# Optimization experiments

Hardware: AMD Instinct MI355X
Metric: run time of the kernel (lower is better)

## Reference

```python
import jax, jax.numpy as jnp
import numpy as np

B, T, F, H = 32768, 64, 8, 16
NUM_LABELS, OUT_WIN = 4, 8
FC1_OUT = F * T          # 512
FC2_OUT = NUM_LABELS * OUT_WIN  # 32


def _lstm_relu(x_tbf, W, U, b):
    """Keras LSTM with activation='relu', recurrent_activation='sigmoid'.
    x_tbf: [T, B, F_in]. Returns all hidden states [T, B, H].
    Gate order in Keras kernel: i, f, c, o."""
    Bv = x_tbf.shape[1]
    h0 = jnp.zeros((Bv, H), x_tbf.dtype)
    c0 = jnp.zeros((Bv, H), x_tbf.dtype)

    def step(carry, xt):
        h, c = carry
        z = xt @ W + h @ U + b  # [B, 4H]
        i, f, g, o = jnp.split(z, 4, axis=-1)
        i = jax.nn.sigmoid(i)
        f = jax.nn.sigmoid(f)
        o = jax.nn.sigmoid(o)
        c = f * c + i * jax.nn.relu(g)
        h = o * jax.nn.relu(c)
        return (h, c), h

    _, hs = jax.lax.scan(step, (h0, c0), x_tbf)
    return hs  # [T, B, H]


def setup_inputs() -> dict:
    key = jax.random.key(0)
    ks = jax.random.split(key, 12)
    s = lambda fan_in: 1.0 / np.sqrt(fan_in)
    x = jax.random.normal(ks[0], (B, T, F), dtype=jnp.float32)
    W1 = jax.random.normal(ks[1], (F, 4 * H), dtype=jnp.float32) * s(F)
    U1 = jax.random.normal(ks[2], (H, 4 * H), dtype=jnp.float32) * s(H)
    b1 = jnp.zeros((4 * H,), jnp.float32)
    W2 = jax.random.normal(ks[3], (H, 4 * H), dtype=jnp.float32) * s(H)
    U2 = jax.random.normal(ks[4], (H, 4 * H), dtype=jnp.float32) * s(H)
    b2 = jnp.zeros((4 * H,), jnp.float32)
    Wfc1 = jax.random.normal(ks[5], (H, FC1_OUT), dtype=jnp.float32) * s(H)
    bfc1 = jnp.zeros((FC1_OUT,), jnp.float32)
    Wfc2 = jax.random.normal(ks[6], (FC1_OUT, FC2_OUT), dtype=jnp.float32) * s(FC1_OUT)
    bfc2 = jnp.zeros((FC2_OUT,), jnp.float32)
    return {"x": x, "W1": W1, "U1": U1, "b1": b1, "W2": W2, "U2": U2,
            "b2": b2, "Wfc1": Wfc1, "bfc1": bfc1, "Wfc2": Wfc2, "bfc2": bfc2}


def reference(x, W1, U1, b1, W2, U2, b2, Wfc1, bfc1, Wfc2, bfc2):
    x_tbf = jnp.transpose(x, (1, 0, 2))        # [T, B, F]
    h1 = _lstm_relu(x_tbf, W1, U1, b1)         # [T, B, H] (return_sequences=True)
    h2 = _lstm_relu(h1, W2, U2, b2)[-1]        # [B, H] (return_sequences=False)
    # Dropout is identity at inference (training=False).
    y = jax.nn.relu(h2 @ Wfc1 + bfc1)          # [B, 512]
    y = y @ Wfc2 + bfc2                        # [B, 32]
    return y
```

## Files before the change

### kernel.cpp

```cpp
#include <hip/hip_runtime.h>
#include <stdint.h>


#define NT 64
#define NF 8

typedef __attribute__((ext_vector_type(8))) short bf16x8;
typedef __attribute__((ext_vector_type(4))) float f32x4;

#define MFMA16 __builtin_amdgcn_mfma_f32_16x16x32_bf16

static __device__ __forceinline__ short f2bf(float f) {
  uint32_t u = __float_as_uint(f);
  u += 0x7FFFu + ((u >> 16) & 1u);
  return (short)(u >> 16);
}
static __device__ __forceinline__ float bf2f(short s) {
  return __uint_as_float(((uint32_t)(uint16_t)s) << 16);
}
static __device__ __forceinline__ void split_hl(float f, short& hi, short& lo) {
  short h = f2bf(f);
  hi = h;
  lo = f2bf(f - bf2f(h));
}
static __device__ __forceinline__ float sigmoidf_(float v) {
  return __builtin_amdgcn_rcpf(1.0f + __expf(-v));
}
static __device__ __forceinline__ void lds_fence() {
  asm volatile("s_waitcnt lgkmcnt(0)" ::: "memory");
  __builtin_amdgcn_sched_barrier(0);
}

__global__ __launch_bounds__(256, 2) void lstm_fused(
    const float* __restrict__ x,
    const float* __restrict__ W1, const float* __restrict__ U1, const float* __restrict__ b1,
    const float* __restrict__ W2, const float* __restrict__ U2, const float* __restrict__ b2,
    const float* __restrict__ Wfc1, const float* __restrict__ bfc1,
    const float* __restrict__ Wfc2, const float* __restrict__ bfc2,
    float* __restrict__ out)
{
  const int tid  = threadIdx.x;
  const int lane = tid & 63;
  const int wv   = tid >> 6;
  const int col  = lane & 15;
  const int g    = lane >> 4;
  const int ho   = (g & 1) * 8;
  const int base = (blockIdx.x * 4 + wv) * 16;

  __shared__ __align__(16) short lds_all[4][1536 + 1280];
  short* const s1_hi = &lds_all[wv][0];
  short* const s1_lo = s1_hi + 384;
  short* const s2_hi = s1_hi + 768;
  short* const s2_lo = s1_hi + 1152;
  short* const c_hi  = s1_hi + 1536;
  short* const c_lo  = s1_hi + 1536 + 640;

  for (int i = lane; i < 1536; i += 64) s1_hi[i] = 0;
  lds_fence();

  bf16x8 B1a[4], B2a[4], B1b[4], B2b[4];
#pragma unroll
  for (int n = 0; n < 4; ++n) {
    const int c = 16 * n + col;
#pragma unroll
    for (int j = 0; j < 8; ++j) {
      const int k = 8 * g + j;
      short h, l;
      if (k < 8)       { split_hl(W1[k * 64 + c], h, l);        B1a[n][j] = h; B2a[n][j] = l; }
      else if (k < 16) { split_hl(W1[(k - 8) * 64 + c], h, l);  B1a[n][j] = h; B2a[n][j] = 0; }
      else             { split_hl(U1[(k - 16) * 64 + c], h, l); B1a[n][j] = h; B2a[n][j] = l; }
      short h2, l2;
      if (k < 16) split_hl(W2[k * 64 + c], h2, l2);
      else        split_hl(U2[(k - 16) * 64 + c], h2, l2);
      B1b[n][j] = h2; B2b[n][j] = l2;
    }
  }

  float bias1[4], bias2[4];
#pragma unroll
  for (int n = 0; n < 4; ++n) { bias1[n] = b1[16 * n + col]; bias2[n] = b2[16 * n + col]; }

  f32x4 c1 = {0.f, 0.f, 0.f, 0.f};
  f32x4 c2 = {0.f, 0.f, 0.f, 0.f};

  const float* xrow = x + (size_t)(base + col) * (NT * NF);
  const short* const l2ph = (g < 2) ? s1_hi : s2_hi;
  const short* const l2pl = (g < 2) ? s1_lo : s2_lo;

  for (int t = 0; t < NT; ++t) {
    f32x4 xa = *(const f32x4*)(xrow + t * NF);
    f32x4 xb = *(const f32x4*)(xrow + t * NF + 4);
    bf16x8 xh8, xl8;
#pragma unroll
    for (int j = 0; j < 4; ++j) {
      short h, l;
      split_hl(xa[j], h, l); xh8[j] = h;     xl8[j] = l;
      split_hl(xb[j], h, l); xh8[4 + j] = h; xl8[4 + j] = l;
    }
    bf16x8 hh = *(const bf16x8*)(s1_hi + col * 24 + ho);
    bf16x8 hl = *(const bf16x8*)(s1_lo + col * 24 + ho);
    bf16x8 A1, A3;
#pragma unroll
    for (int j = 0; j < 8; ++j) {
      A1[j] = (g == 0) ? xh8[j] : ((g == 1) ? xl8[j] : hh[j]);
      A3[j] = (g < 2) ? (short)0 : hl[j];
    }
    f32x4 z[4];
#pragma unroll
    for (int n = 0; n < 4; ++n) {
      f32x4 zi = {bias1[n], bias1[n], bias1[n], bias1[n]};
      zi = MFMA16(A1, B1a[n], zi, 0, 0, 0);
      zi = MFMA16(A1, B2a[n], zi, 0, 0, 0);
      zi = MFMA16(A3, B1a[n], zi, 0, 0, 0);
      z[n] = zi;
    }
    f32x4 h1v;
#pragma unroll
    for (int r = 0; r < 4; ++r) {
      float ig = sigmoidf_(z[0][r]);
      float fg = sigmoidf_(z[1][r]);
      float gg = fmaxf(z[2][r], 0.f);
      float og = sigmoidf_(z[3][r]);
      float cc = fg * c1[r] + ig * gg;
      c1[r] = cc;
      h1v[r] = og * fmaxf(cc, 0.f);
    }
#pragma unroll
    for (int r = 0; r < 4; ++r) {
      short h, l; split_hl(h1v[r], h, l);
      s1_hi[(4 * g + r) * 24 + col] = h;
      s1_lo[(4 * g + r) * 24 + col] = l;
    }
    lds_fence();

    bf16x8 A1c = *(const bf16x8*)(l2ph + col * 24 + ho);
    bf16x8 A3c = *(const bf16x8*)(l2pl + col * 24 + ho);
    f32x4 y[4];
#pragma unroll
    for (int n = 0; n < 4; ++n) {
      f32x4 yi = {bias2[n], bias2[n], bias2[n], bias2[n]};
      yi = MFMA16(A1c, B1b[n], yi, 0, 0, 0);
      yi = MFMA16(A1c, B2b[n], yi, 0, 0, 0);
      yi = MFMA16(A3c, B1b[n], yi, 0, 0, 0);
      y[n] = yi;
    }
    f32x4 h2v;
#pragma unroll
    for (int r = 0; r < 4; ++r) {
      float ig = sigmoidf_(y[0][r]);
      float fg = sigmoidf_(y[1][r]);
      float gg = fmaxf(y[2][r], 0.f);
      float og = sigmoidf_(y[3][r]);
      float cc = fg * c2[r] + ig * gg;
      c2[r] = cc;
      h2v[r] = og * fmaxf(cc, 0.f);
    }
#pragma unroll
    for (int r = 0; r < 4; ++r) {
      short h, l; split_hl(h2v[r], h, l);
      s2_hi[(4 * g + r) * 24 + col] = h;
      s2_lo[(4 * g + r) * 24 + col] = l;
    }
    lds_fence();
  }

  const short* pf = (g < 2) ? s2_hi : s2_lo;
  bf16x8 Afc = *(const bf16x8*)(pf + col * 24 + ho);

  f32x4 acc2[2];
#pragma unroll
  for (int nn = 0; nn < 2; ++nn) {
    float bb = bfc2[16 * nn + col];
    f32x4 a = {bb, bb, bb, bb};
    acc2[nn] = a;
  }

  for (int kc = 0; kc < 16; ++kc) {
#pragma unroll
    for (int s = 0; s < 2; ++s) {
      const int c = 16 * (2 * kc + s) + col;
      bf16x8 Bh, Bl;
#pragma unroll
      for (int j = 0; j < 8; ++j) {
        short h, l;
        split_hl(Wfc1[((8 * g + j) & 15) * 512 + c], h, l);
        Bh[j] = h; Bl[j] = l;
      }
      float bb = bfc1[c];
      f32x4 acc = {bb, bb, bb, bb};
      acc = MFMA16(Afc, Bh, acc, 0, 0, 0);
      acc = MFMA16(Afc, Bl, acc, 0, 0, 0);
#pragma unroll
      for (int r = 0; r < 4; ++r) {
        short h, l;
        split_hl(fmaxf(acc[r], 0.f), h, l);
        c_hi[(4 * g + r) * 40 + 16 * s + col] = h;
        c_lo[(4 * g + r) * 40 + 16 * s + col] = l;
      }
    }
    lds_fence();
    bf16x8 Ah = *(const bf16x8*)(c_hi + col * 40 + 8 * g);
    bf16x8 Al = *(const bf16x8*)(c_lo + col * 40 + 8 * g);
#pragma unroll
    for (int nn = 0; nn < 2; ++nn) {
      bf16x8 Bh, Bl;
#pragma unroll
      for (int j = 0; j < 8; ++j) {
        short h, l;
        split_hl(Wfc2[(size_t)(32 * kc + 8 * g + j) * 32 + 16 * nn + col], h, l);
        Bh[j] = h; Bl[j] = l;
      }
      acc2[nn] = MFMA16(Ah, Bh, acc2[nn], 0, 0, 0);
      acc2[nn] = MFMA16(Al, Bh, acc2[nn], 0, 0, 0);
      acc2[nn] = MFMA16(Ah, Bl, acc2[nn], 0, 0, 0);
    }
    lds_fence();
  }

#pragma unroll
  for (int nn = 0; nn < 2; ++nn)
#pragma unroll
    for (int r = 0; r < 4; ++r)
      out[(size_t)(base + 4 * g + r) * 32 + 16 * nn + col] = acc2[nn][r];
}

extern "C" void kernel_launch(void* const* d_in, const int* in_sizes, int n_in,
                              void* d_out, int out_size, void* d_ws, size_t ws_size,
                              hipStream_t stream) {
  const float* x    = (const float*)d_in[0];
  const float* W1   = (const float*)d_in[1];
  const float* U1   = (const float*)d_in[2];
  const float* b1   = (const float*)d_in[3];
  const float* W2   = (const float*)d_in[4];
  const float* U2   = (const float*)d_in[5];
  const float* b2   = (const float*)d_in[6];
  const float* Wfc1 = (const float*)d_in[7];
  const float* bfc1 = (const float*)d_in[8];
  const float* Wfc2 = (const float*)d_in[9];
  const float* bfc2 = (const float*)d_in[10];

  lstm_fused<<<dim3(512), dim3(256), 0, stream>>>(
      x, W1, U1, b1, W2, U2, b2, Wfc1, bfc1, Wfc2, bfc2, (float*)d_out);
}
```

Baseline: 244.1 us.

## Skew both LSTM layers into one step loop and prefetch x and FC weights

Each loop iteration now computes layer-1 step t alongside layer-2 step t-1 from a shared LDS layout, with a prologue and an epilogue for the edge steps. This replaces two dependent LDS fence round-trips per timestep with one and gives the MFMA chains of the two layers room to overlap. The next timestep's x row and the next FC1/FC2 weight chunk are loaded one iteration ahead to hide global latency, and the sched_barrier after each fence is removed. Costs are more registers for the prefetch buffers and a more intricate LDS layout; a dead set of layer-2 MFMAs is left in the loop, which the compiler is expected to drop.

Result: slower. 252.1 us (+3.3%).

```diff
diff --git a/kernel.cpp b/kernel.cpp
--- a/kernel.cpp
+++ b/kernel.cpp
@@ -28,7 +28,9 @@
 }
 static __device__ __forceinline__ void lds_fence() {
   asm volatile("s_waitcnt lgkmcnt(0)" ::: "memory");
-  __builtin_amdgcn_sched_barrier(0);
+}
+static __device__ __forceinline__ void cbar() {
+  asm volatile("" ::: "memory");
 }
 
 __global__ __launch_bounds__(256, 2) void lstm_fused(
@@ -44,19 +46,23 @@
   const int wv   = tid >> 6;
   const int col  = lane & 15;
   const int g    = lane >> 4;
-  const int ho   = (g & 1) * 8;
   const int base = (blockIdx.x * 4 + wv) * 16;
 
-  __shared__ __align__(16) short lds_all[4][1536 + 1280];
-  short* const s1_hi = &lds_all[wv][0];
-  short* const s1_lo = s1_hi + 384;
-  short* const s2_hi = s1_hi + 768;
-  short* const s2_lo = s1_hi + 1152;
-  short* const c_hi  = s1_hi + 1536;
-  short* const c_lo  = s1_hi + 1536 + 640;
-
-  for (int i = lane; i < 1536; i += 64) s1_hi[i] = 0;
-  lds_fence();
+  __shared__ __align__(16) short lds_all[4][4 * 512 + 2 * 640];
+  short* const l1h = &lds_all[wv][0];
+  short* const l1l = l1h + 512;
+  short* const l2h = l1h + 1024;
+  short* const l2l = l1h + 1536;
+  short* const cfh = l1h + 2048;
+  short* const cfl = l1h + 2048 + 640;
+
+  {
+    int4 z4 = make_int4(0, 0, 0, 0);
+    int4* p = (int4*)l1h;
+#pragma unroll
+    for (int i = 0; i < 4; ++i) p[lane + 64 * i] = z4;
+  }
+  cbar();
 
   bf16x8 B1a[4], B2a[4], B1b[4], B2b[4];
 #pragma unroll
@@ -76,20 +82,25 @@
     }
   }
 
-  float bias1[4], bias2[4];
-#pragma unroll
-  for (int n = 0; n < 4; ++n) { bias1[n] = b1[16 * n + col]; bias2[n] = b2[16 * n + col]; }
-
-  f32x4 c1 = {0.f, 0.f, 0.f, 0.f};
-  f32x4 c2 = {0.f, 0.f, 0.f, 0.f};
+  f32x4 bias1v[4], bias2v[4];
+#pragma unroll
+  for (int n = 0; n < 4; ++n) {
+    float b1s = b1[16 * n + col];
+    float b2s = b2[16 * n + col];
+    bias1v[n] = (f32x4){b1s, b1s, b1s, b1s};
+    bias2v[n] = (f32x4){b2s, b2s, b2s, b2s};
+  }
+
+  const short* const aL1h = l1h + col * 32 + 8 * g;
+  const short* const aL1l = l1l + col * 32 + 8 * g;
+  const short* const aL2h = l2h + col * 32 + 8 * g;
+  const short* const aL2l = l2l + col * 32 + 8 * g;
 
   const float* xrow = x + (size_t)(base + col) * (NT * NF);
-  const short* const l2ph = (g < 2) ? s1_hi : s2_hi;
-  const short* const l2pl = (g < 2) ? s1_lo : s2_lo;
-
-  for (int t = 0; t < NT; ++t) {
-    f32x4 xa = *(const f32x4*)(xrow + t * NF);
-    f32x4 xb = *(const f32x4*)(xrow + t * NF + 4);
+
+  {
+    f32x4 xa = *(const f32x4*)(xrow);
+    f32x4 xb = *(const f32x4*)(xrow + 4);
     bf16x8 xh8, xl8;
 #pragma unroll
     for (int j = 0; j < 4; ++j) {
@@ -97,24 +108,29 @@
       split_hl(xa[j], h, l); xh8[j] = h;     xl8[j] = l;
       split_hl(xb[j], h, l); xh8[4 + j] = h; xl8[4 + j] = l;
     }
-    bf16x8 hh = *(const bf16x8*)(s1_hi + col * 24 + ho);
-    bf16x8 hl = *(const bf16x8*)(s1_lo + col * 24 + ho);
-    bf16x8 A1, A3;
-#pragma unroll
-    for (int j = 0; j < 8; ++j) {
-      A1[j] = (g == 0) ? xh8[j] : ((g == 1) ? xl8[j] : hh[j]);
-      A3[j] = (g < 2) ? (short)0 : hl[j];
-    }
+    if (g == 0)      *(bf16x8*)(l1h + col * 32)     = xh8;
+    else if (g == 1) *(bf16x8*)(l1h + col * 32 + 8) = xl8;
+  }
+  lds_fence();
+
+  f32x4 c1 = {0.f, 0.f, 0.f, 0.f};
+  f32x4 c2 = {0.f, 0.f, 0.f, 0.f};
+  f32x4 h1v, h2v;
+
+  {
+    bf16x8 A1 = *(const bf16x8*)aL1h;
+    bf16x8 A3 = *(const bf16x8*)aL1l;
+    f32x4 xa = *(const f32x4*)(xrow + NF);
+    f32x4 xb = *(const f32x4*)(xrow + NF + 4);
     f32x4 z[4];
 #pragma unroll
     for (int n = 0; n < 4; ++n) {
-      f32x4 zi = {bias1[n], bias1[n], bias1[n], bias1[n]};
+      f32x4 zi = bias1v[n];
       zi = MFMA16(A1, B1a[n], zi, 0, 0, 0);
       zi = MFMA16(A1, B2a[n], zi, 0, 0, 0);
       zi = MFMA16(A3, B1a[n], zi, 0, 0, 0);
       z[n] = zi;
     }
-    f32x4 h1v;
 #pragma unroll
     for (int r = 0; r < 4; ++r) {
       float ig = sigmoidf_(z[0][r]);
@@ -125,26 +141,69 @@
       c1[r] = cc;
       h1v[r] = og * fmaxf(cc, 0.f);
     }
-#pragma unroll
-    for (int r = 0; r < 4; ++r) {
-      short h, l; split_hl(h1v[r], h, l);
-      s1_hi[(4 * g + r) * 24 + col] = h;
-      s1_lo[(4 * g + r) * 24 + col] = l;
-    }
-    lds_fence();
-
-    bf16x8 A1c = *(const bf16x8*)(l2ph + col * 24 + ho);
-    bf16x8 A3c = *(const bf16x8*)(l2pl + col * 24 + ho);
-    f32x4 y[4];
+    cbar();
+    bf16x8 xh8, xl8;
+#pragma unroll
+    for (int j = 0; j < 4; ++j) {
+      short h, l;
+      split_hl(xa[j], h, l); xh8[j] = h;     xl8[j] = l;
+      split_hl(xb[j], h, l); xh8[4 + j] = h; xl8[4 + j] = l;
+    }
+    if (g == 0)      *(bf16x8*)(l1h + col * 32)     = xh8;
+    else if (g == 1) *(bf16x8*)(l1h + col * 32 + 8) = xl8;
+#pragma unroll
+    for (int r = 0; r < 4; ++r) {
+      short hh_, ll_; split_hl(h1v[r], hh_, ll_);
+      const int row = 4 * g + r;
+      l1h[row * 32 + 16 + col] = hh_;
+      l1l[row * 32 + 16 + col] = ll_;
+      l2h[row * 32 + col]      = hh_;
+      l2l[row * 32 + col]      = ll_;
+    }
+    lds_fence();
+  }
+
+  for (int i = 1; i < NT; ++i) {
+    bf16x8 A1  = *(const bf16x8*)aL1h;
+    bf16x8 A3  = *(const bf16x8*)aL1l;
+    bf16x8 A1c = *(const bf16x8*)aL2h;
+    bf16x8 A3c = *(const bf16x8*)aL2l;
+    const int tn = (i + 1 < NT) ? (i + 1) : (NT - 1);
+    f32x4 xa = *(const f32x4*)(xrow + tn * NF);
+    f32x4 xb = *(const f32x4*)(xrow + tn * NF + 4);
+
+    f32x4 z[4], y[4];
 #pragma unroll
     for (int n = 0; n < 4; ++n) {
-      f32x4 yi = {bias2[n], bias2[n], bias2[n], bias2[n]};
+      f32x4 zi = bias1v[n];
+      zi = MFMA16(A1, B1a[n], zi, 0, 0, 0);
+      zi = MFMA16(A1, B2a[n], zi, 0, 0, 0);
+      zi = MFMA16(A3, B1a[n], zi, 0, 0, 0);
+      z[n] = zi;
+      f32x4 yi = bias2v[n];
+      yi = MFMA16(A1c, B1b[n], yi, 0, 0, 0);
+      yi = MFMA16(A1c, B2b[n], yi, 0, 0, 0);
+      yi = MFMA16(A3c, B2b[n], yi, 0, 0, 0);
+      y[n] = yi;
+    }
+#pragma unroll
+    for (int n = 0; n < 4; ++n) {
+      f32x4 yi = bias2v[n];
       yi = MFMA16(A1c, B1b[n], yi, 0, 0, 0);
       yi = MFMA16(A1c, B2b[n], yi, 0, 0, 0);
       yi = MFMA16(A3c, B1b[n], yi, 0, 0, 0);
       y[n] = yi;
     }
-    f32x4 h2v;
+#pragma unroll
+    for (int r = 0; r < 4; ++r) {
+      float ig = sigmoidf_(z[0][r]);
+      float fg = sigmoidf_(z[1][r]);
+      float gg = fmaxf(z[2][r], 0.f);
+      float og = sigmoidf_(z[3][r]);
+      float cc = fg * c1[r] + ig * gg;
+      c1[r] = cc;
+      h1v[r] = og * fmaxf(cc, 0.f);
+    }
 #pragma unroll
     for (int r = 0; r < 4; ++r) {
       float ig = sigmoidf_(y[0][r]);
@@ -155,59 +214,130 @@
       c2[r] = cc;
       h2v[r] = og * fmaxf(cc, 0.f);
     }
-#pragma unroll
-    for (int r = 0; r < 4; ++r) {
-      short h, l; split_hl(h2v[r], h, l);
-      s2_hi[(4 * g + r) * 24 + col] = h;
-      s2_lo[(4 * g + r) * 24 + col] = l;
-    }
-    lds_fence();
-  }
-
-  const short* pf = (g < 2) ? s2_hi : s2_lo;
-  bf16x8 Afc = *(const bf16x8*)(pf + col * 24 + ho);
+    cbar();
+    bf16x8 xh8, xl8;
+#pragma unroll
+    for (int j = 0; j < 4; ++j) {
+      short h, l;
+      split_hl(xa[j], h, l); xh8[j] = h;     xl8[j] = l;
+      split_hl(xb[j], h, l); xh8[4 + j] = h; xl8[4 + j] = l;
+    }
+    if (g == 0)      *(bf16x8*)(l1h + col * 32)     = xh8;
+    else if (g == 1) *(bf16x8*)(l1h + col * 32 + 8) = xl8;
+#pragma unroll
+    for (int r = 0; r < 4; ++r) {
+      short hh_, ll_; split_hl(h1v[r], hh_, ll_);
+      const int row = 4 * g + r;
+      l1h[row * 32 + 16 + col] = hh_;
+      l1l[row * 32 + 16 + col] = ll_;
+      l2h[row * 32 + col]      = hh_;
+      l2l[row * 32 + col]      = ll_;
+    }
+#pragma unroll
+    for (int r = 0; r < 4; ++r) {
+      short hh_, ll_; split_hl(h2v[r], hh_, ll_);
+      const int row = 4 * g + r;
+      l2h[row * 32 + 16 + col] = hh_;
+      l2l[row * 32 + 16 + col] = ll_;
+    }
+    lds_fence();
+  }
+
+  {
+    bf16x8 A1c = *(const bf16x8*)aL2h;
+    bf16x8 A3c = *(const bf16x8*)aL2l;
+    f32x4 y[4];
+#pragma unroll
+    for (int n = 0; n < 4; ++n) {
+      f32x4 yi = bias2v[n];
+      yi = MFMA16(A1c, B1b[n], yi, 0, 0, 0);
+      yi = MFMA16(A1c, B2b[n], yi, 0, 0, 0);
+      yi = MFMA16(A3c, B1b[n], yi, 0, 0, 0);
+      y[n] = yi;
+    }
+#pragma unroll
+    for (int r = 0; r < 4; ++r) {
+      float ig = sigmoidf_(y[0][r]);
+      float fg = sigmoidf_(y[1][r]);
+      float gg = fmaxf(y[2][r], 0.f);
+      float og = sigmoidf_(y[3][r]);
+      float cc = fg * c2[r] + ig * gg;
+      c2[r] = cc;
+      h2v[r] = og * fmaxf(cc, 0.f);
+    }
+    cbar();
+#pragma unroll
+    for (int r = 0; r < 4; ++r) {
+      short hh_, ll_; split_hl(h2v[r], hh_, ll_);
+      const int row = 4 * g + r;
+      l2h[row * 32 + 16 + col] = hh_;
+      l2l[row * 32 + 16 + col] = ll_;
+    }
+    lds_fence();
+  }
+
+  const short* afp = ((g < 2) ? l2h : l2l) + col * 32 + 16 + (g & 1) * 8;
+  bf16x8 Afc = *(const bf16x8*)afp;
 
   f32x4 acc2[2];
 #pragma unroll
   for (int nn = 0; nn < 2; ++nn) {
     float bb = bfc2[16 * nn + col];
-    f32x4 a = {bb, bb, bb, bb};
-    acc2[nn] = a;
+    acc2[nn] = (f32x4){bb, bb, bb, bb};
+  }
+
+  float cw1[16], cw2[16];
+#pragma unroll
+  for (int j = 0; j < 8; ++j) {
+    const int kr = (8 * g + j) & 15;
+    cw1[j]     = Wfc1[kr * 512 + col];
+    cw1[8 + j] = Wfc1[kr * 512 + 16 + col];
+    cw2[j]     = Wfc2[(8 * g + j) * 32 + col];
+    cw2[8 + j] = Wfc2[(8 * g + j) * 32 + 16 + col];
   }
 
   for (int kc = 0; kc < 16; ++kc) {
+    const int kn = (kc < 15) ? kc + 1 : 15;
+    float nw1[16], nw2[16];
+#pragma unroll
+    for (int j = 0; j < 8; ++j) {
+      const int kr = (8 * g + j) & 15;
+      nw1[j]     = Wfc1[kr * 512 + 32 * kn + col];
+      nw1[8 + j] = Wfc1[kr * 512 + 32 * kn + 16 + col];
+      nw2[j]     = Wfc2[(size_t)(32 * kn + 8 * g + j) * 32 + col];
+      nw2[8 + j] = Wfc2[(size_t)(32 * kn + 8 * g + j) * 32 + 16 + col];
+    }
 #pragma unroll
     for (int s = 0; s < 2; ++s) {
-      const int c = 16 * (2 * kc + s) + col;
       bf16x8 Bh, Bl;
 #pragma unroll
       for (int j = 0; j < 8; ++j) {
         short h, l;
-        split_hl(Wfc1[((8 * g + j) & 15) * 512 + c], h, l);
+        split_hl(cw1[8 * s + j], h, l);
         Bh[j] = h; Bl[j] = l;
       }
-      float bb = bfc1[c];
-      f32x4 acc = {bb, bb, bb, bb};
+      float bb = bfc1[32 * kc + 16 * s + col];
+      f32x4 acc = (f32x4){bb, bb, bb, bb};
       acc = MFMA16(Afc, Bh, acc, 0, 0, 0);
       acc = MFMA16(Afc, Bl, acc, 0, 0, 0);
 #pragma unroll
       for (int r = 0; r < 4; ++r) {
         short h, l;
         split_hl(fmaxf(acc[r], 0.f), h, l);
-        c_hi[(4 * g + r) * 40 + 16 * s + col] = h;
-        c_lo[(4 * g + r) * 40 + 16 * s + col] = l;
+        cfh[(4 * g + r) * 40 + 16 * s + col] = h;
+        cfl[(4 * g + r) * 40 + 16 * s + col] = l;
       }
     }
     lds_fence();
-    bf16x8 Ah = *(const bf16x8*)(c_hi + col * 40 + 8 * g);
-    bf16x8 Al = *(const bf16x8*)(c_lo + col * 40 + 8 * g);
+    bf16x8 Ah = *(const bf16x8*)(cfh + col * 40 + 8 * g);
+    bf16x8 Al = *(const bf16x8*)(cfl + col * 40 + 8 * g);
 #pragma unroll
     for (int nn = 0; nn < 2; ++nn) {
       bf16x8 Bh, Bl;
 #pragma unroll
       for (int j = 0; j < 8; ++j) {
         short h, l;
-        split_hl(Wfc2[(size_t)(32 * kc + 8 * g + j) * 32 + 16 * nn + col], h, l);
+        split_hl(cw2[8 * nn + j], h, l);
         Bh[j] = h; Bl[j] = l;
       }
       acc2[nn] = MFMA16(Ah, Bh, acc2[nn], 0, 0, 0);
@@ -215,6 +345,8 @@
       acc2[nn] = MFMA16(Ah, Bl, acc2[nn], 0, 0, 0);
     }
     lds_fence();
+#pragma unroll
+    for (int q = 0; q < 16; ++q) { cw1[q] = nw1[q]; cw2[q] = nw2[q]; }
   }
 
 #pragma unroll
```

## Skew LSTM layers, transpose MFMA operands, pass hidden state via bpermute

Applied to the files above, without the earlier changes.

Swaps the MFMA operand roles so the weights are the A operand and hidden state the B operand, giving gate outputs per batch column. It skews layer 2 by one timestep so both layers' MFMAs in a step are independent and can interleave. Hidden states now move between lanes with ds_bpermute instead of LDS stores, loads and fences, and x is prefetched one step ahead. It adds a peeled final layer-2 step and extra packing logic, which raises register pressure.

Result: faster. 235.7 us (-3.4%).

```diff
diff --git a/kernel.cpp b/kernel.cpp
--- a/kernel.cpp
+++ b/kernel.cpp
@@ -7,28 +7,45 @@
 
 typedef __attribute__((ext_vector_type(8))) short bf16x8;
 typedef __attribute__((ext_vector_type(4))) float f32x4;
+typedef __attribute__((ext_vector_type(2))) unsigned int u32x2;
+typedef __attribute__((ext_vector_type(4))) unsigned int u32x4;
 
 #define MFMA16 __builtin_amdgcn_mfma_f32_16x16x32_bf16
 
-static __device__ __forceinline__ short f2bf(float f) {
+static __device__ __forceinline__ uint32_t bfraw(float f) {
   uint32_t u = __float_as_uint(f);
-  u += 0x7FFFu + ((u >> 16) & 1u);
-  return (short)(u >> 16);
-}
-static __device__ __forceinline__ float bf2f(short s) {
-  return __uint_as_float(((uint32_t)(uint16_t)s) << 16);
+  return u + 0x7FFFu + ((u >> 16) & 1u);
+}
+static __device__ __forceinline__ float hipart(uint32_t raw) {
+  return __uint_as_float(raw & 0xFFFF0000u);
+}
+static __device__ __forceinline__ void pack_hl(float a, float b,
+                                               uint32_t& hi, uint32_t& lo) {
+  uint32_t ra = bfraw(a), rb = bfraw(b);
+  hi = (rb & 0xFFFF0000u) | (ra >> 16);
+  float la = a - hipart(ra);
+  float lb = b - hipart(rb);
+  uint32_t rla = bfraw(la), rlb = bfraw(rb == 0u ? 0.f : lb);
+  rlb = bfraw(lb);
+  lo = (rlb & 0xFFFF0000u) | (rla >> 16);
 }
 static __device__ __forceinline__ void split_hl(float f, short& hi, short& lo) {
-  short h = f2bf(f);
-  hi = h;
-  lo = f2bf(f - bf2f(h));
+  uint32_t r = bfraw(f);
+  hi = (short)(r >> 16);
+  float res = f - hipart(r);
+  lo = (short)(bfraw(res) >> 16);
 }
 static __device__ __forceinline__ float sigmoidf_(float v) {
   return __builtin_amdgcn_rcpf(1.0f + __expf(-v));
 }
+static __device__ __forceinline__ bf16x8 asbf(u32x4 w) {
+  union { u32x4 u; bf16x8 b; } c; c.u = w; return c.b;
+}
+static __device__ __forceinline__ uint32_t bperm(int addr, uint32_t v) {
+  return (uint32_t)__builtin_amdgcn_ds_bpermute(addr, (int)v);
+}
 static __device__ __forceinline__ void lds_fence() {
   asm volatile("s_waitcnt lgkmcnt(0)" ::: "memory");
-  __builtin_amdgcn_sched_barrier(0);
 }
 
 __global__ __launch_bounds__(256, 2) void lstm_fused(
@@ -44,19 +61,11 @@
   const int wv   = tid >> 6;
   const int col  = lane & 15;
   const int g    = lane >> 4;
-  const int ho   = (g & 1) * 8;
   const int base = (blockIdx.x * 4 + wv) * 16;
 
-  __shared__ __align__(16) short lds_all[4][1536 + 1280];
-  short* const s1_hi = &lds_all[wv][0];
-  short* const s1_lo = s1_hi + 384;
-  short* const s2_hi = s1_hi + 768;
-  short* const s2_lo = s1_hi + 1152;
-  short* const c_hi  = s1_hi + 1536;
-  short* const c_lo  = s1_hi + 1536 + 640;
-
-  for (int i = lane; i < 1536; i += 64) s1_hi[i] = 0;
-  lds_fence();
+  __shared__ __align__(16) short cf[4][2][512];
+  short* const cfh = &cf[wv][0][0];
+  short* const cfl = &cf[wv][1][0];
 
   bf16x8 B1a[4], B2a[4], B1b[4], B2b[4];
 #pragma unroll
@@ -76,45 +85,65 @@
     }
   }
 
-  float bias1[4], bias2[4];
-#pragma unroll
-  for (int n = 0; n < 4; ++n) { bias1[n] = b1[16 * n + col]; bias2[n] = b2[16 * n + col]; }
+  f32x4 bias1v[4], bias2v[4];
+#pragma unroll
+  for (int n = 0; n < 4; ++n) {
+    bias1v[n] = *(const f32x4*)(b1 + 16 * n + 4 * g);
+    bias2v[n] = *(const f32x4*)(b2 + 16 * n + 4 * g);
+  }
+
+  const int addrA = ((g & 1) * 32 + col) * 4;
+  const int addrB = addrA + 64;
 
   f32x4 c1 = {0.f, 0.f, 0.f, 0.f};
   f32x4 c2 = {0.f, 0.f, 0.f, 0.f};
+  uint32_t h1ph[4] = {0,0,0,0}, h1pl[4] = {0,0,0,0};
+  uint32_t h2ph[4] = {0,0,0,0}, h2pl[4] = {0,0,0,0};
 
   const float* xrow = x + (size_t)(base + col) * (NT * NF);
-  const short* const l2ph = (g < 2) ? s1_hi : s2_hi;
-  const short* const l2pl = (g < 2) ? s1_lo : s2_lo;
-
-  for (int t = 0; t < NT; ++t) {
-    f32x4 xa = *(const f32x4*)(xrow + t * NF);
-    f32x4 xb = *(const f32x4*)(xrow + t * NF + 4);
-    bf16x8 xh8, xl8;
-#pragma unroll
-    for (int j = 0; j < 4; ++j) {
-      short h, l;
-      split_hl(xa[j], h, l); xh8[j] = h;     xl8[j] = l;
-      split_hl(xb[j], h, l); xh8[4 + j] = h; xl8[4 + j] = l;
-    }
-    bf16x8 hh = *(const bf16x8*)(s1_hi + col * 24 + ho);
-    bf16x8 hl = *(const bf16x8*)(s1_lo + col * 24 + ho);
-    bf16x8 A1, A3;
-#pragma unroll
-    for (int j = 0; j < 8; ++j) {
-      A1[j] = (g == 0) ? xh8[j] : ((g == 1) ? xl8[j] : hh[j]);
-      A3[j] = (g < 2) ? (short)0 : hl[j];
-    }
-    f32x4 z[4];
+  f32x4 xa = *(const f32x4*)(xrow);
+  f32x4 xb = *(const f32x4*)(xrow + 4);
+
+  for (int i = 0; i < NT; ++i) {
+    u32x4 l2b1w, l2b3w;
+#pragma unroll
+    for (int q = 0; q < 4; ++q) {
+      l2b1w[q] = (g < 2) ? h1ph[q] : h2ph[q];
+      l2b3w[q] = (g < 2) ? h1pl[q] : h2pl[q];
+    }
+    uint32_t xh[4], xl[4];
+    pack_hl(xa[0], xa[1], xh[0], xl[0]);
+    pack_hl(xa[2], xa[3], xh[1], xl[1]);
+    pack_hl(xb[0], xb[1], xh[2], xl[2]);
+    pack_hl(xb[2], xb[3], xh[3], xl[3]);
+    if (i + 1 < NT) {
+      xa = *(const f32x4*)(xrow + (i + 1) * NF);
+      xb = *(const f32x4*)(xrow + (i + 1) * NF + 4);
+    }
+    u32x4 l1b1w, l1b3w;
+#pragma unroll
+    for (int q = 0; q < 4; ++q) {
+      uint32_t xw = (g == 0) ? xh[q] : xl[q];
+      l1b1w[q] = (g < 2) ? xw : h1ph[q];
+      l1b3w[q] = (g < 2) ? 0u : h1pl[q];
+    }
+    bf16x8 L1B1 = asbf(l1b1w), L1B3 = asbf(l1b3w);
+    bf16x8 L2B1 = asbf(l2b1w), L2B3 = asbf(l2b3w);
+
+    f32x4 z[4], y[4];
 #pragma unroll
     for (int n = 0; n < 4; ++n) {
-      f32x4 zi = {bias1[n], bias1[n], bias1[n], bias1[n]};
-      zi = MFMA16(A1, B1a[n], zi, 0, 0, 0);
-      zi = MFMA16(A1, B2a[n], zi, 0, 0, 0);
-      zi = MFMA16(A3, B1a[n], zi, 0, 0, 0);
+      f32x4 zi = MFMA16(B1a[n], L1B1, bias1v[n], 0, 0, 0);
+      zi = MFMA16(B2a[n], L1B1, zi, 0, 0, 0);
+      zi = MFMA16(B1a[n], L1B3, zi, 0, 0, 0);
       z[n] = zi;
-    }
-    f32x4 h1v;
+      f32x4 yi = MFMA16(B1b[n], L2B1, bias2v[n], 0, 0, 0);
+      yi = MFMA16(B2b[n], L2B1, yi, 0, 0, 0);
+      yi = MFMA16(B1b[n], L2B3, yi, 0, 0, 0);
+      y[n] = yi;
+    }
+
+    f32x4 h1v, h2v;
 #pragma unroll
     for (int r = 0; r < 4; ++r) {
       float ig = sigmoidf_(z[0][r]);
@@ -125,23 +154,55 @@
       c1[r] = cc;
       h1v[r] = og * fmaxf(cc, 0.f);
     }
-#pragma unroll
-    for (int r = 0; r < 4; ++r) {
-      short h, l; split_hl(h1v[r], h, l);
-      s1_hi[(4 * g + r) * 24 + col] = h;
-      s1_lo[(4 * g + r) * 24 + col] = l;
-    }
-    lds_fence();
-
-    bf16x8 A1c = *(const bf16x8*)(l2ph + col * 24 + ho);
-    bf16x8 A3c = *(const bf16x8*)(l2pl + col * 24 + ho);
+    if (i != 0) {
+#pragma unroll
+      for (int r = 0; r < 4; ++r) {
+        float ig = sigmoidf_(y[0][r]);
+        float fg = sigmoidf_(y[1][r]);
+        float gg = fmaxf(y[2][r], 0.f);
+        float og = sigmoidf_(y[3][r]);
+        float cc = fg * c2[r] + ig * gg;
+        c2[r] = cc;
+        h2v[r] = og * fmaxf(cc, 0.f);
+      }
+    } else {
+      h2v = (f32x4){0.f, 0.f, 0.f, 0.f};
+    }
+
+    {
+      uint32_t p01h, p01l, p23h, p23l;
+      pack_hl(h1v[0], h1v[1], p01h, p01l);
+      pack_hl(h1v[2], h1v[3], p23h, p23l);
+      h1ph[0] = bperm(addrA, p01h); h1ph[1] = bperm(addrA, p23h);
+      h1ph[2] = bperm(addrB, p01h); h1ph[3] = bperm(addrB, p23h);
+      h1pl[0] = bperm(addrA, p01l); h1pl[1] = bperm(addrA, p23l);
+      h1pl[2] = bperm(addrB, p01l); h1pl[3] = bperm(addrB, p23l);
+    }
+    {
+      uint32_t p01h, p01l, p23h, p23l;
+      pack_hl(h2v[0], h2v[1], p01h, p01l);
+      pack_hl(h2v[2], h2v[3], p23h, p23l);
+      h2ph[0] = bperm(addrA, p01h); h2ph[1] = bperm(addrA, p23h);
+      h2ph[2] = bperm(addrB, p01h); h2ph[3] = bperm(addrB, p23h);
+      h2pl[0] = bperm(addrA, p01l); h2pl[1] = bperm(addrA, p23l);
+      h2pl[2] = bperm(addrB, p01l); h2pl[3] = bperm(addrB, p23l);
+    }
+  }
+
+  {
+    u32x4 b1w, b3w;
+#pragma unroll
+    for (int q = 0; q < 4; ++q) {
+      b1w[q] = (g < 2) ? h1ph[q] : h2ph[q];
+      b3w[q] = (g < 2) ? h1pl[q] : h2pl[q];
+    }
+    bf16x8 L2B1 = asbf(b1w), L2B3 = asbf(b3w);
     f32x4 y[4];
 #pragma unroll
     for (int n = 0; n < 4; ++n) {
-      f32x4 yi = {bias2[n], bias2[n], bias2[n], bias2[n]};
-      yi = MFMA16(A1c, B1b[n], yi, 0, 0, 0);
-      yi = MFMA16(A1c, B2b[n], yi, 0, 0, 0);
-      yi = MFMA16(A3c, B1b[n], yi, 0, 0, 0);
+      f32x4 yi = MFMA16(B1b[n], L2B1, bias2v[n], 0, 0, 0);
+      yi = MFMA16(B2b[n], L2B1, yi, 0, 0, 0);
+      yi = MFMA16(B1b[n], L2B3, yi, 0, 0, 0);
       y[n] = yi;
     }
     f32x4 h2v;
@@ -155,73 +216,67 @@
       c2[r] = cc;
       h2v[r] = og * fmaxf(cc, 0.f);
     }
-#pragma unroll
-    for (int r = 0; r < 4; ++r) {
-      short h, l; split_hl(h2v[r], h, l);
-      s2_hi[(4 * g + r) * 24 + col] = h;
-      s2_lo[(4 * g + r) * 24 + col] = l;
+    uint32_t p01h, p01l, p23h, p23l;
+    pack_hl(h2v[0], h2v[1], p01h, p01l);
+    pack_hl(h2v[2], h2v[3], p23h, p23l);
+    h2ph[0] = bperm(addrA, p01h); h2ph[1] = bperm(addrA, p23h);
+    h2ph[2] = bperm(addrB, p01h); h2ph[3] = bperm(addrB, p23h);
+    h2pl[0] = bperm(addrA, p01l); h2pl[1] = bperm(addrA, p23l);
+    h2pl[2] = bperm(addrB, p01l); h2pl[3] = bperm(addrB, p23l);
+  }
+
+  u32x4 bwf;
+#pragma unroll
+  for (int q = 0; q < 4; ++q) bwf[q] = (g < 2) ? h2ph[q] : h2pl[q];
+  bf16x8 Bfc = asbf(bwf);
+
+  f32x4 acc2[2];
+#pragma unroll
+  for (int nn = 0; nn < 2; ++nn)
+    acc2[nn] = *(const f32x4*)(bfc2 + 16 * nn + 4 * g);
+
+  for (int kc = 0; kc < 16; ++kc) {
+#pragma unroll
+    for (int t = 0; t < 2; ++t) {
+      const int mt = 2 * kc + t;
+      bf16x8 A1h, A1l;
+#pragma unroll
+      for (int j = 0; j < 8; ++j) {
+        float w = Wfc1[((8 * g + j) & 15) * 512 + 16 * mt + col];
+        short h, l; split_hl(w, h, l);
+        A1h[j] = h; A1l[j] = l;
+      }
+      f32x4 bv = *(const f32x4*)(bfc1 + 16 * mt + 4 * g);
+      f32x4 acc = MFMA16(A1h, Bfc, bv, 0, 0, 0);
+      acc = MFMA16(A1l, Bfc, acc, 0, 0, 0);
+      uint32_t q01h, q01l, q23h, q23l;
+      pack_hl(fmaxf(acc[0], 0.f), fmaxf(acc[1], 0.f), q01h, q01l);
+      pack_hl(fmaxf(acc[2], 0.f), fmaxf(acc[3], 0.f), q23h, q23l);
+      *(u32x2*)((char*)cfh + col * 64 + 32 * t + 8 * g) = (u32x2){q01h, q23h};
+      *(u32x2*)((char*)cfl + col * 64 + 32 * t + 8 * g) = (u32x2){q01l, q23l};
     }
     lds_fence();
-  }
-
-  const short* pf = (g < 2) ? s2_hi : s2_lo;
-  bf16x8 Afc = *(const bf16x8*)(pf + col * 24 + ho);
-
-  f32x4 acc2[2];
-#pragma unroll
-  for (int nn = 0; nn < 2; ++nn) {
-    float bb = bfc2[16 * nn + col];
-    f32x4 a = {bb, bb, bb, bb};
-    acc2[nn] = a;
-  }
-
-  for (int kc = 0; kc < 16; ++kc) {
-#pragma unroll
-    for (int s = 0; s < 2; ++s) {
-      const int c = 16 * (2 * kc + s) + col;
-      bf16x8 Bh, Bl;
+    bf16x8 Bh = *(const bf16x8*)((char*)cfh + col * 64 + 16 * g);
+    bf16x8 Bl = *(const bf16x8*)((char*)cfl + col * 64 + 16 * g);
+#pragma unroll
+    for (int nn = 0; nn < 2; ++nn) {
+      bf16x8 A2h, A2l;
 #pragma unroll
       for (int j = 0; j < 8; ++j) {
-        short h, l;
-        split_hl(Wfc1[((8 * g + j) & 15) * 512 + c], h, l);
-        Bh[j] = h; Bl[j] = l;
+        float w = Wfc2[(size_t)(32 * kc + 8 * g + j) * 32 + 16 * nn + col];
+        short h, l; split_hl(w, h, l);
+        A2h[j] = h; A2l[j] = l;
       }
-      float bb = bfc1[c];
-      f32x4 acc = {bb, bb, bb, bb};
-      acc = MFMA16(Afc, Bh, acc, 0, 0, 0);
-      acc = MFMA16(Afc, Bl, acc, 0, 0, 0);
-#pragma unroll
-      for (int r = 0; r < 4; ++r) {
-        short h, l;
-        split_hl(fmaxf(acc[r], 0.f), h, l);
-        c_hi[(4 * g + r) * 40 + 16 * s + col] = h;
-        c_lo[(4 * g + r) * 40 + 16 * s + col] = l;
-      }
+      acc2[nn] = MFMA16(A2h, Bh, acc2[nn], 0, 0, 0);
+      acc2[nn] = MFMA16(A2h, Bl, acc2[nn], 0, 0, 0);
+      acc2[nn] = MFMA16(A2l, Bh, acc2[nn], 0, 0, 0);
     }
     lds_fence();
-    bf16x8 Ah = *(const bf16x8*)(c_hi + col * 40 + 8 * g);
-    bf16x8 Al = *(const bf16x8*)(c_lo + col * 40 + 8 * g);
-#pragma unroll
-    for (int nn = 0; nn < 2; ++nn) {
-      bf16x8 Bh, Bl;
-#pragma unroll
-      for (int j = 0; j < 8; ++j) {
-        short h, l;
-        split_hl(Wfc2[(size_t)(32 * kc + 8 * g + j) * 32 + 16 * nn + col], h, l);
-        Bh[j] = h; Bl[j] = l;
-      }
-      acc2[nn] = MFMA16(Ah, Bh, acc2[nn], 0, 0, 0);
-      acc2[nn] = MFMA16(Al, Bh, acc2[nn], 0, 0, 0);
-      acc2[nn] = MFMA16(Ah, Bl, acc2[nn], 0, 0, 0);
-    }
-    lds_fence();
   }
 
 #pragma unroll
   for (int nn = 0; nn < 2; ++nn)
-#pragma unroll
-    for (int r = 0; r < 4; ++r)
-      out[(size_t)(base + 4 * g + r) * 32 + 16 * nn + col] = acc2[nn][r];
+    *(f32x4*)(out + (size_t)(base + col) * 32 + 16 * nn + 4 * g) = acc2[nn];
 }
 
 extern "C" void kernel_launch(void* const* d_in, const int* in_sizes, int n_in,
```
